# Performance work log

Hardware: AMD Instinct MI355X
Metric: run time of the kernel (lower is better)

Reference implementation:

```python
import jax, jax.numpy as jnp
import numpy as np

HEADS = 16
LOCAL_ATTN_CTX = 128  # band half-width for attn_mode='local'
NEG = -1e9


def setup_inputs() -> dict:
    key = jax.random.key(0)
    kq, kk, kv = jax.random.split(key, 3)
    B, N, D = 1, 2048, 1024
    q = jax.random.normal(kq, (B, N, D), dtype=jnp.float32)
    k = jax.random.normal(kk, (B, N, D), dtype=jnp.float32)
    v = jax.random.normal(kv, (B, N, D), dtype=jnp.float32)
    return {"q": q, "k": k, "v": v}


def _split_heads(x, h):
    # [B, N, D] -> [B, H, N, Dh]
    B, N, D = x.shape
    return x.reshape(B, N, h, D // h).transpose(0, 2, 1, 3)


def _local_mask(n, ctx):
    # band mask: 1 where |i-j| <= ctx, matching sum of diag ones in torch code
    idx = jnp.arange(n)
    return (jnp.abs(idx[:, None] - idx[None, :]) <= ctx).astype(jnp.float32)


def reference(q, k, v):
    B, N, D = q.shape
    qh = _split_heads(q, HEADS)  # [B,H,N,Dh]
    kh = _split_heads(k, HEADS)
    vh = _split_heads(v, HEADS)
    dh = D // HEADS
    scale = 1.0 / np.sqrt(dh).astype(np.float32)
    mask = _local_mask(N, LOCAL_ATTN_CTX)  # [N,N]
    w = jnp.einsum('bhnd,bhmd->bhnm', qh, kh) * scale
    w = w * mask + NEG * (1.0 - mask)
    w = jax.nn.softmax(w, axis=-1)
    a = jnp.einsum('bhnm,bhmd->bhnd', w, vh)  # [B,H,N,Dh]
    # merge heads: [B,H,N,Dh] -> [B,N,D]
    return a.transpose(0, 2, 1, 3).reshape(B, N, D)
```

## Files before the change

kernel.cpp:

```cpp
#include <hip/hip_runtime.h>

#define HEADS 16
#define SEQ_N 2048
#define DMODEL 1024
#define DH 64
#define CTX 128
#define QBLK 64
#define KBLK 32
#define LDK 72
#define LDV 36
#define KELEM (KBLK * LDK)
#define VELEM (DH * LDV)
#define MSTR 17

typedef __attribute__((ext_vector_type(8))) short short8;
typedef __attribute__((ext_vector_type(4))) float f32x4;
typedef __attribute__((ext_vector_type(4))) unsigned int u32x4;

__device__ __forceinline__ unsigned rne2(float lo, float hi) {
    union { float f; unsigned u; } a, b; a.f = lo; b.f = hi;
    return __builtin_amdgcn_perm(b.u + 0x8000u, a.u + 0x8000u, 0x07060302u);
}
__device__ __forceinline__ u32x4 pack8w(float4 a, float4 b) {
    u32x4 w;
    w.x = rne2(a.x, a.y); w.y = rne2(a.z, a.w);
    w.z = rne2(b.x, b.y); w.w = rne2(b.z, b.w);
    return w;
}
__device__ __forceinline__ short8 mk_frag(const ushort* p0, const ushort* p1) {
    union { unsigned long long u[2]; short8 s; } cv;
    cv.u[0] = *(const unsigned long long*)p0;
    cv.u[1] = *(const unsigned long long*)p1;
    return cv.s;
}
__device__ __forceinline__ float fexp2(float x) {
#if __has_builtin(__builtin_amdgcn_exp2f)
    return __builtin_amdgcn_exp2f(x);
#else
    return exp2f(x);
#endif
}

__global__ __launch_bounds__(512) void sattn_w15(
    const float* __restrict__ qm, const float* __restrict__ km,
    const float* __restrict__ vm, float* __restrict__ out)
{
    union Smem {
        struct { ushort kt[2][2][KELEM]; ushort vt[2][2][VELEM]; } tl;
        float mbuf[4][64][MSTR];
    };
    __shared__ Smem sm;

    const int h     = blockIdx.x;
    const int qbase = blockIdx.y * QBLK;
    const int t     = threadIdx.x;
    const int wave  = t >> 6;
    const int lane  = t & 63;
    const int half  = wave & 1;
    const int qgi   = wave >> 1;
    const int lq    = lane & 15;
    const int g     = lane >> 4;
    const int iq    = qbase + qgi * 16 + lq;
    const int q0    = qbase + qgi * 16;

    const int jlo  = max(0, qbase - CTX);
    const int jhi  = min(SEQ_N - 1, qbase + QBLK - 1 + CTX);
    const int nch  = (jhi - jlo + 1) >> 5;
    const int nchH = nch >> 1;
    const int jbs[2] = { jlo, jlo + nchH * KBLK };

    const float qs = 0.18033688011112042f;
    short8 qf[2];
    {
        const float* qrow = qm + (size_t)iq * DMODEL + h * DH;
        #pragma unroll
        for (int kc = 0; kc < 2; ++kc) {
            float4 f0 = *(const float4*)(qrow + kc * 32 + g * 4);
            float4 f1 = *(const float4*)(qrow + kc * 32 + 16 + g * 4);
            f0.x *= qs; f0.y *= qs; f0.z *= qs; f0.w *= qs;
            f1.x *= qs; f1.y *= qs; f1.z *= qs; f1.w *= qs;
            union { u32x4 w; short8 s; } u;
            u.w = pack8w(f0, f1);
            qf[kc] = u.s;
        }
    }

    const int shf  = t >> 8;
    const int srow = (t >> 3) & 31;
    const int sdg  = t & 7;
    const int vkey = srow ^ (sdg << 2);

    float4 pk0, pk1, pv0, pv1;
    auto prefetch = [&](int it) {
        const int j = jbs[shf] + it * KBLK + srow;
        const float* kp = km + (size_t)j * DMODEL + h * DH + sdg * 8;
        const float* vp = vm + (size_t)j * DMODEL + h * DH + sdg * 8;
        pk0 = ((const float4*)kp)[0]; pk1 = ((const float4*)kp)[1];
        pv0 = ((const float4*)vp)[0]; pv1 = ((const float4*)vp)[1];
    };
    auto stage = [&](int buf) {
        *(u32x4*)&sm.tl.kt[buf][shf][srow * LDK + sdg * 8] = pack8w(pk0, pk1);
        union { u32x4 w; ushort u[8]; } vb;
        vb.w = pack8w(pv0, pv1);
        #pragma unroll
        for (int e = 0; e < 8; ++e)
            sm.tl.vt[buf][shf][(sdg * 8 + e) * LDV + vkey] = vb.u[e];
    };

    f32x4 oacc[4];
    #pragma unroll
    for (int dt = 0; dt < 4; ++dt) oacc[dt] = (f32x4){0.f, 0.f, 0.f, 0.f};
    float lsum = 0.f;

    prefetch(0);
    stage(0);
    __syncthreads();

    for (int it = 0; it < nchH; ++it) {
        const int cur = it & 1;
        const bool more = (it + 1 < nchH);
        if (more) prefetch(it + 1);

        __builtin_amdgcn_s_setprio(1);
        f32x4 st0 = (f32x4){0.f, 0.f, 0.f, 0.f};
        f32x4 st1 = (f32x4){0.f, 0.f, 0.f, 0.f};
        #pragma unroll
        for (int kc = 0; kc < 2; ++kc) {
            const ushort* kr0 = &sm.tl.kt[cur][half][lq * LDK + kc * 32 + g * 4];
            const ushort* kr1 = &sm.tl.kt[cur][half][(16 + lq) * LDK + kc * 32 + g * 4];
            st0 = __builtin_amdgcn_mfma_f32_16x16x32_bf16(
                mk_frag(kr0, kr0 + 16), qf[kc], st0, 0, 0, 0);
            st1 = __builtin_amdgcn_mfma_f32_16x16x32_bf16(
                mk_frag(kr1, kr1 + 16), qf[kc], st1, 0, 0, 0);
        }

        const int jc = jbs[half] + it * KBLK;
        float p0[4], p1[4];
        if (jc >= q0 - 113 && jc <= q0 + 97) {
            #pragma unroll
            for (int r = 0; r < 4; ++r) {
                p0[r] = fexp2(st0[r]);
                p1[r] = fexp2(st1[r]);
            }
        } else {
            const int dbase = jc - iq + CTX;
            #pragma unroll
            for (int r = 0; r < 4; ++r) {
                const int loc0 = g * 4 + r;
                const float s0 = ((unsigned)(dbase + loc0)      <= 2u * CTX) ? st0[r] : -1.0e30f;
                const float s1 = ((unsigned)(dbase + loc0 + 16) <= 2u * CTX) ? st1[r] : -1.0e30f;
                p0[r] = fexp2(s0);
                p1[r] = fexp2(s1);
            }
        }
        float psum = 0.f;
        #pragma unroll
        for (int r = 0; r < 4; ++r) psum += p0[r] + p1[r];
        lsum += psum;
        union { unsigned w[4]; short8 s8; } pf;
        pf.w[0] = rne2(p0[0], p0[1]); pf.w[1] = rne2(p0[2], p0[3]);
        pf.w[2] = rne2(p1[0], p1[1]); pf.w[3] = rne2(p1[2], p1[3]);

        #pragma unroll
        for (int dt = 0; dt < 4; ++dt) {
            const int c = (dt * 2 + (lq >> 3)) & 7;
            const ushort* vrow = &sm.tl.vt[cur][half][(dt * 16 + lq) * LDV];
            const ushort* vr0 = vrow + ((g ^ c) << 2);
            const ushort* vr1 = vrow + (((g + 4) ^ c) << 2);
            oacc[dt] = __builtin_amdgcn_mfma_f32_16x16x32_bf16(
                mk_frag(vr0, vr1), pf.s8, oacc[dt], 0, 0, 0);
        }
        __builtin_amdgcn_s_setprio(0);

        if (more) stage(cur ^ 1);
        __syncthreads();
    }

    lsum += __shfl_xor(lsum, 16);
    lsum += __shfl_xor(lsum, 32);

    if (half == 1) {
        float* mb = sm.mbuf[qgi][lane];
        #pragma unroll
        for (int dt = 0; dt < 4; ++dt) {
            #pragma unroll
            for (int r = 0; r < 4; ++r) mb[dt * 4 + r] = oacc[dt][r];
        }
        mb[16] = lsum;
    }
    __syncthreads();
    if (half == 0) {
        const float* mb = sm.mbuf[qgi][lane];
        #pragma unroll
        for (int dt = 0; dt < 4; ++dt) {
            #pragma unroll
            for (int r = 0; r < 4; ++r) oacc[dt][r] += mb[dt * 4 + r];
        }
        const float inv = 1.0f / (lsum + mb[16]);
        float* orow = out + (size_t)iq * DMODEL + h * DH;
        #pragma unroll
        for (int dt = 0; dt < 4; ++dt) {
            float4 o;
            o.x = oacc[dt][0] * inv; o.y = oacc[dt][1] * inv;
            o.z = oacc[dt][2] * inv; o.w = oacc[dt][3] * inv;
            *(float4*)&orow[dt * 16 + g * 4] = o;
        }
    }
}

extern "C" void kernel_launch(void* const* d_in, const int* in_sizes, int n_in,
                              void* d_out, int out_size, void* d_ws, size_t ws_size,
                              hipStream_t stream) {
    const float* q = (const float*)d_in[0];
    const float* k = (const float*)d_in[1];
    const float* v = (const float*)d_in[2];
    float* out = (float*)d_out;

    dim3 grid(HEADS, SEQ_N / QBLK);
    dim3 block(512);
    sattn_w15<<<grid, block, 0, stream>>>(q, k, v, out);
}
```

Measured before the change: 16.23 us.

## Split key range across four waves per query group with 1024-thread blocks

Each 16-query group now has four waves instead of two, each covering a quarter of the key chunks. Block size doubles to 1024 threads and the partial outputs are merged through shared memory across three partner waves. The aim is to shorten each wave's serial key loop and raise parallelism in this small grid of 512 blocks. The cost is more shared memory, a heavier reduction, and idle waves when the chunk count is not divisible by four, since all waves still hit every barrier.

```diff
diff --git a/kernel.cpp b/kernel.cpp
--- a/kernel.cpp
+++ b/kernel.cpp
@@ -41,13 +41,13 @@
 #endif
 }
 
-__global__ __launch_bounds__(512) void sattn_w15(
+__global__ __launch_bounds__(1024, 8) void sattn_w17(
     const float* __restrict__ qm, const float* __restrict__ km,
     const float* __restrict__ vm, float* __restrict__ out)
 {
     union Smem {
-        struct { ushort kt[2][2][KELEM]; ushort vt[2][2][VELEM]; } tl;
-        float mbuf[4][64][MSTR];
+        struct { ushort kt[2][4][KELEM]; ushort vt[2][4][VELEM]; } tl;
+        float mbuf[4][3][64][MSTR];
     };
     __shared__ Smem sm;
 
@@ -56,8 +56,8 @@
     const int t     = threadIdx.x;
     const int wave  = t >> 6;
     const int lane  = t & 63;
-    const int half  = wave & 1;
-    const int qgi   = wave >> 1;
+    const int qtr   = wave & 3;
+    const int qgi   = wave >> 2;
     const int lq    = lane & 15;
     const int g     = lane >> 4;
     const int iq    = qbase + qgi * 16 + lq;
@@ -66,8 +66,15 @@
     const int jlo  = max(0, qbase - CTX);
     const int jhi  = min(SEQ_N - 1, qbase + QBLK - 1 + CTX);
     const int nch  = (jhi - jlo + 1) >> 5;
-    const int nchH = nch >> 1;
-    const int jbs[2] = { jlo, jlo + nchH * KBLK };
+    const int nq0 = (nch + 3) >> 2, nq1 = (nch + 2) >> 2;
+    const int nq2 = (nch + 1) >> 2, nq3 = nch >> 2;
+    const int jb0 = jlo;
+    const int jb1 = jb0 + nq0 * KBLK;
+    const int jb2 = jb1 + nq1 * KBLK;
+    const int jb3 = jb2 + nq2 * KBLK;
+    const int itmax = nq0;
+    const int myn  = (qtr == 0) ? nq0 : (qtr == 1) ? nq1 : (qtr == 2) ? nq2 : nq3;
+    const int jmyb = (qtr == 0) ? jb0 : (qtr == 1) ? jb1 : (qtr == 2) ? jb2 : jb3;
 
     const float qs = 0.18033688011112042f;
     short8 qf[2];
@@ -85,26 +92,29 @@
         }
     }
 
-    const int shf  = t >> 8;
+    const int sqt  = t >> 8;
     const int srow = (t >> 3) & 31;
     const int sdg  = t & 7;
     const int vkey = srow ^ (sdg << 2);
+    const int jstb = (sqt == 0) ? jb0 : (sqt == 1) ? jb1 : (sqt == 2) ? jb2 : jb3;
+    const int nst  = (sqt == 0) ? nq0 : (sqt == 1) ? nq1 : (sqt == 2) ? nq2 : nq3;
 
     float4 pk0, pk1, pv0, pv1;
     auto prefetch = [&](int it) {
-        const int j = jbs[shf] + it * KBLK + srow;
+        const int c = (it < nst) ? it : 0;
+        const int j = jstb + c * KBLK + srow;
         const float* kp = km + (size_t)j * DMODEL + h * DH + sdg * 8;
         const float* vp = vm + (size_t)j * DMODEL + h * DH + sdg * 8;
         pk0 = ((const float4*)kp)[0]; pk1 = ((const float4*)kp)[1];
         pv0 = ((const float4*)vp)[0]; pv1 = ((const float4*)vp)[1];
     };
     auto stage = [&](int buf) {
-        *(u32x4*)&sm.tl.kt[buf][shf][srow * LDK + sdg * 8] = pack8w(pk0, pk1);
+        *(u32x4*)&sm.tl.kt[buf][sqt][srow * LDK + sdg * 8] = pack8w(pk0, pk1);
         union { u32x4 w; ushort u[8]; } vb;
         vb.w = pack8w(pv0, pv1);
         #pragma unroll
         for (int e = 0; e < 8; ++e)
-            sm.tl.vt[buf][shf][(sdg * 8 + e) * LDV + vkey] = vb.u[e];
+            sm.tl.vt[buf][sqt][(sdg * 8 + e) * LDV + vkey] = vb.u[e];
     };
 
     f32x4 oacc[4];
@@ -116,61 +126,63 @@
     stage(0);
     __syncthreads();
 
-    for (int it = 0; it < nchH; ++it) {
+    for (int it = 0; it < itmax; ++it) {
         const int cur = it & 1;
-        const bool more = (it + 1 < nchH);
+        const bool more = (it + 1 < itmax);
         if (more) prefetch(it + 1);
 
-        __builtin_amdgcn_s_setprio(1);
-        f32x4 st0 = (f32x4){0.f, 0.f, 0.f, 0.f};
-        f32x4 st1 = (f32x4){0.f, 0.f, 0.f, 0.f};
-        #pragma unroll
-        for (int kc = 0; kc < 2; ++kc) {
-            const ushort* kr0 = &sm.tl.kt[cur][half][lq * LDK + kc * 32 + g * 4];
-            const ushort* kr1 = &sm.tl.kt[cur][half][(16 + lq) * LDK + kc * 32 + g * 4];
-            st0 = __builtin_amdgcn_mfma_f32_16x16x32_bf16(
-                mk_frag(kr0, kr0 + 16), qf[kc], st0, 0, 0, 0);
-            st1 = __builtin_amdgcn_mfma_f32_16x16x32_bf16(
-                mk_frag(kr1, kr1 + 16), qf[kc], st1, 0, 0, 0);
-        }
-
-        const int jc = jbs[half] + it * KBLK;
-        float p0[4], p1[4];
-        if (jc >= q0 - 113 && jc <= q0 + 97) {
-            #pragma unroll
-            for (int r = 0; r < 4; ++r) {
-                p0[r] = fexp2(st0[r]);
-                p1[r] = fexp2(st1[r]);
-            }
-        } else {
-            const int dbase = jc - iq + CTX;
-            #pragma unroll
-            for (int r = 0; r < 4; ++r) {
-                const int loc0 = g * 4 + r;
-                const float s0 = ((unsigned)(dbase + loc0)      <= 2u * CTX) ? st0[r] : -1.0e30f;
-                const float s1 = ((unsigned)(dbase + loc0 + 16) <= 2u * CTX) ? st1[r] : -1.0e30f;
-                p0[r] = fexp2(s0);
-                p1[r] = fexp2(s1);
-            }
-        }
-        float psum = 0.f;
-        #pragma unroll
-        for (int r = 0; r < 4; ++r) psum += p0[r] + p1[r];
-        lsum += psum;
-        union { unsigned w[4]; short8 s8; } pf;
-        pf.w[0] = rne2(p0[0], p0[1]); pf.w[1] = rne2(p0[2], p0[3]);
-        pf.w[2] = rne2(p1[0], p1[1]); pf.w[3] = rne2(p1[2], p1[3]);
-
-        #pragma unroll
-        for (int dt = 0; dt < 4; ++dt) {
-            const int c = (dt * 2 + (lq >> 3)) & 7;
-            const ushort* vrow = &sm.tl.vt[cur][half][(dt * 16 + lq) * LDV];
-            const ushort* vr0 = vrow + ((g ^ c) << 2);
-            const ushort* vr1 = vrow + (((g + 4) ^ c) << 2);
-            oacc[dt] = __builtin_amdgcn_mfma_f32_16x16x32_bf16(
-                mk_frag(vr0, vr1), pf.s8, oacc[dt], 0, 0, 0);
-        }
-        __builtin_amdgcn_s_setprio(0);
+        if (it < myn) {
+            __builtin_amdgcn_s_setprio(1);
+            f32x4 st0 = (f32x4){0.f, 0.f, 0.f, 0.f};
+            f32x4 st1 = (f32x4){0.f, 0.f, 0.f, 0.f};
+            #pragma unroll
+            for (int kc = 0; kc < 2; ++kc) {
+                const ushort* kr0 = &sm.tl.kt[cur][qtr][lq * LDK + kc * 32 + g * 4];
+                const ushort* kr1 = &sm.tl.kt[cur][qtr][(16 + lq) * LDK + kc * 32 + g * 4];
+                st0 = __builtin_amdgcn_mfma_f32_16x16x32_bf16(
+                    mk_frag(kr0, kr0 + 16), qf[kc], st0, 0, 0, 0);
+                st1 = __builtin_amdgcn_mfma_f32_16x16x32_bf16(
+                    mk_frag(kr1, kr1 + 16), qf[kc], st1, 0, 0, 0);
+            }
+
+            const int jc = jmyb + it * KBLK;
+            float p0[4], p1[4];
+            if (jc >= q0 - 113 && jc <= q0 + 97) {
+                #pragma unroll
+                for (int r = 0; r < 4; ++r) {
+                    p0[r] = fexp2(st0[r]);
+                    p1[r] = fexp2(st1[r]);
+                }
+            } else {
+                const int dbase = jc - iq + CTX;
+                #pragma unroll
+                for (int r = 0; r < 4; ++r) {
+                    const int loc0 = g * 4 + r;
+                    const float s0 = ((unsigned)(dbase + loc0)      <= 2u * CTX) ? st0[r] : -1.0e30f;
+                    const float s1 = ((unsigned)(dbase + loc0 + 16) <= 2u * CTX) ? st1[r] : -1.0e30f;
+                    p0[r] = fexp2(s0);
+                    p1[r] = fexp2(s1);
+                }
+            }
+            float psum = 0.f;
+            #pragma unroll
+            for (int r = 0; r < 4; ++r) psum += p0[r] + p1[r];
+            lsum += psum;
+            union { unsigned w[4]; short8 s8; } pf;
+            pf.w[0] = rne2(p0[0], p0[1]); pf.w[1] = rne2(p0[2], p0[3]);
+            pf.w[2] = rne2(p1[0], p1[1]); pf.w[3] = rne2(p1[2], p1[3]);
+
+            #pragma unroll
+            for (int dt = 0; dt < 4; ++dt) {
+                const int c = (dt * 2 + (lq >> 3)) & 7;
+                const ushort* vrow = &sm.tl.vt[cur][qtr][(dt * 16 + lq) * LDV];
+                const ushort* vr0 = vrow + ((g ^ c) << 2);
+                const ushort* vr1 = vrow + (((g + 4) ^ c) << 2);
+                oacc[dt] = __builtin_amdgcn_mfma_f32_16x16x32_bf16(
+                    mk_frag(vr0, vr1), pf.s8, oacc[dt], 0, 0, 0);
+            }
+            __builtin_amdgcn_s_setprio(0);
+        }
 
         if (more) stage(cur ^ 1);
         __syncthreads();
@@ -179,8 +191,8 @@
     lsum += __shfl_xor(lsum, 16);
     lsum += __shfl_xor(lsum, 32);
 
-    if (half == 1) {
-        float* mb = sm.mbuf[qgi][lane];
+    if (qtr != 0) {
+        float* mb = sm.mbuf[qgi][qtr - 1][lane];
         #pragma unroll
         for (int dt = 0; dt < 4; ++dt) {
             #pragma unroll
@@ -189,14 +201,18 @@
         mb[16] = lsum;
     }
     __syncthreads();
-    if (half == 0) {
-        const float* mb = sm.mbuf[qgi][lane];
-        #pragma unroll
-        for (int dt = 0; dt < 4; ++dt) {
-            #pragma unroll
-            for (int r = 0; r < 4; ++r) oacc[dt][r] += mb[dt * 4 + r];
-        }
-        const float inv = 1.0f / (lsum + mb[16]);
+    if (qtr == 0) {
+        #pragma unroll
+        for (int p = 0; p < 3; ++p) {
+            const float* mb = sm.mbuf[qgi][p][lane];
+            #pragma unroll
+            for (int dt = 0; dt < 4; ++dt) {
+                #pragma unroll
+                for (int r = 0; r < 4; ++r) oacc[dt][r] += mb[dt * 4 + r];
+            }
+            lsum += mb[16];
+        }
+        const float inv = 1.0f / lsum;
         float* orow = out + (size_t)iq * DMODEL + h * DH;
         #pragma unroll
         for (int dt = 0; dt < 4; ++dt) {
@@ -217,6 +233,6 @@
     float* out = (float*)d_out;
 
     dim3 grid(HEADS, SEQ_N / QBLK);
-    dim3 block(512);
-    sattn_w15<<<grid, block, 0, stream>>>(q, k, v, out);
-}
+    dim3 block(1024);
+    sattn_w17<<<grid, block, 0, stream>>>(q, k, v, out);
+}
```

Result: slower. 38.06 us (+134.5%).
